# Performance work log

Measured on AMD Instinct MI355X. Metric: run time of the kernel, lower is better.

The kernel has to match this reference:

```python
import jax, jax.numpy as jnp
import numpy as np

POOL = 7          # pool_size (hard-coded 7x7 bin grid in source)
CROP = 2          # per-bin crop size: 14 // 7
ALPHA = 32        # channels per bin
H = W = 128
C = POOL * POOL * ALPHA  # 1568
NUM_ROIS = 4096


def setup_inputs() -> dict:
    key = jax.random.key(0)
    k_img, k_c, k_s = jax.random.split(key, 3)
    img = jax.random.normal(k_img, (1, H, W, C), dtype=jnp.float32)
    # valid normalized boxes [xmin, ymin, xmax, ymax] in [0, 1]
    cmin = jax.random.uniform(k_c, (1, NUM_ROIS, 2), dtype=jnp.float32) * 0.7
    size = 0.05 + jax.random.uniform(k_s, (1, NUM_ROIS, 2), dtype=jnp.float32) * 0.25
    rois = jnp.concatenate([cmin, cmin + size], axis=-1)  # (1, R, 4)
    return {"img": img, "rois": rois}


def _ps_roi_align(img, rois):
    # img: (1, H, W, 49*alpha) channels-last; rois: (1, R, 4) normalized xyxy
    h, w, c = img.shape[1], img.shape[2], img.shape[3]
    nbins = POOL * POOL
    alpha = c // nbins
    feat = img[0].reshape(h, w, nbins, alpha)  # channel group g <-> bin g

    xmin, ymin, xmax, ymax = (rois[0, :, i] for i in range(4))  # each (R,)
    step_y = (ymax - ymin) / POOL
    step_x = (xmax - xmin) / POOL

    g = jnp.arange(nbins)
    bx = (g // POOL).astype(img.dtype)  # bin order: bin_x outer, bin_y inner
    by = (g % POOL).astype(img.dtype)

    # per-roi per-bin sub-boxes, normalized coords, shape (R, B)
    y1 = ymin[:, None] + by[None, :] * step_y[:, None]
    x1 = xmin[:, None] + bx[None, :] * step_x[:, None]
    y2 = y1 + step_y[:, None]
    x2 = x1 + step_x[:, None]

    # tf.image.crop_and_resize sampling grid for crop size CROP (=2)
    t = jnp.arange(CROP, dtype=img.dtype) / (CROP - 1)  # (CROP,)
    ys = (y1[..., None] + (y2 - y1)[..., None] * t) * (h - 1)  # (R, B, CROP)
    xs = (x1[..., None] + (x2 - x1)[..., None] * t) * (w - 1)

    yg = ys[:, :, :, None]  # (R, B, CROP, 1)
    xg = xs[:, :, None, :]  # (R, B, 1, CROP)
    valid = (yg >= 0) & (yg <= h - 1) & (xg >= 0) & (xg <= w - 1)  # (R,B,CROP,CROP)

    y0f = jnp.floor(yg)
    x0f = jnp.floor(xg)
    wy = (yg - y0f)  # (R, B, CROP, 1)
    wx = (xg - x0f)  # (R, B, 1, CROP)

    y0 = jnp.clip(y0f.astype(jnp.int32), 0, h - 1)
    y1i = jnp.clip(y0 + 1, 0, h - 1)
    x0 = jnp.clip(x0f.astype(jnp.int32), 0, w - 1)
    x1i = jnp.clip(x0 + 1, 0, w - 1)

    bidx = g[None, :, None, None]  # (1, B, 1, 1) -> broadcasts with index grids

    def gather(yi, xi):
        yi, xi, bi = jnp.broadcast_arrays(yi, xi, bidx)
        return feat[yi, xi, bi]  # (R, B, CROP, CROP, alpha)

    val = (gather(y0, x0) * ((1 - wy) * (1 - wx))[..., None]
           + gather(y0, x1i) * ((1 - wy) * wx)[..., None]
           + gather(y1i, x0) * (wy * (1 - wx))[..., None]
           + gather(y1i, x1i) * (wy * wx)[..., None])
    val = jnp.where(valid[..., None], val, jnp.zeros((), img.dtype))

    pooled = val.max(axis=(2, 3))  # max over the CROPxCROP crop -> (R, B, alpha)
    return pooled.reshape(1, rois.shape[1], POOL, POOL, alpha)


def reference(img, rois):
    return _ps_roi_align(img, rois)
```

## Files before the change

### kernel.cpp

```cpp
#include <hip/hip_runtime.h>

#define POOLK 7
#define NBINS 49
#define ALPHA 32
#define C4N   8
#define HH    128
#define WW    128
#define NUM_ROIS 4096
#define F4_PER_PIX (NBINS * C4N)

__global__ __launch_bounds__(256) void psroi_align_kernel(
    const float* __restrict__ img,
    const float4* __restrict__ rois4,
    float4* __restrict__ out4)
{
    const int tid = blockIdx.x * blockDim.x + threadIdx.x;
    const int c4  = tid & (C4N - 1);
    const int rg  = tid >> 3;
    const int g   = rg % NBINS;
    const int roi = rg / NBINS;

    const float4 r = rois4[roi];

    const float step_x = (r.z - r.x) * (1.0f / POOLK);
    const float step_y = (r.w - r.y) * (1.0f / POOLK);

    const int p = g / POOLK;
    const int q = g % POOLK;

    const float x1 = r.x + (float)p * step_x;
    const float y1 = r.y + (float)q * step_y;

    const float scale = (float)(HH - 1);
    float ys[2], xs[2];
    ys[0] = y1 * scale;
    ys[1] = (y1 + step_y) * scale;
    xs[0] = x1 * scale;
    xs[1] = (x1 + step_x) * scale;

    float wy[2], wx[2];
    bool  vy[2], vx[2];
    int   yrow[4], xcol[4];
    #pragma unroll
    for (int s = 0; s < 2; ++s) {
        const float yg = ys[s];
        vy[s] = (yg >= 0.0f) && (yg <= (float)(HH - 1));
        const float y0f = floorf(yg);
        wy[s] = yg - y0f;
        int y0 = min(max((int)y0f, 0), HH - 1);
        yrow[2 * s]     = y0;
        yrow[2 * s + 1] = min(y0 + 1, HH - 1);

        const float xg = xs[s];
        vx[s] = (xg >= 0.0f) && (xg <= (float)(WW - 1));
        const float x0f = floorf(xg);
        wx[s] = xg - x0f;
        int x0 = min(max((int)x0f, 0), WW - 1);
        xcol[2 * s]     = x0;
        xcol[2 * s + 1] = min(x0 + 1, WW - 1);
    }

    const float4* __restrict__ feat = (const float4*)img;
    const int gbase = g * C4N + c4;

    int rowoff[4], coloff[4];
    #pragma unroll
    for (int i = 0; i < 4; ++i) {
        rowoff[i] = yrow[i] * (WW * F4_PER_PIX) + gbase;
        coloff[i] = xcol[i] * F4_PER_PIX;
    }

    float4 ld[16];
    #pragma unroll
    for (int rr = 0; rr < 4; ++rr) {
        #pragma unroll
        for (int cc = 0; cc < 4; ++cc) {
            ld[rr * 4 + cc] = feat[rowoff[rr] + coloff[cc]];
        }
    }

    float4 vmax;
    vmax.x = -INFINITY; vmax.y = -INFINITY; vmax.z = -INFINITY; vmax.w = -INFINITY;

    #pragma unroll
    for (int sy = 0; sy < 2; ++sy) {
        #pragma unroll
        for (int sx = 0; sx < 2; ++sx) {
            const float w11 = wy[sy] * wx[sx];
            const float w10 = wy[sy] - w11;
            const float w01 = wx[sx] - w11;
            const float w00 = 1.0f - wy[sy] - wx[sx] + w11;

            const float4 v00 = ld[(2 * sy)     * 4 + (2 * sx)];
            const float4 v01 = ld[(2 * sy)     * 4 + (2 * sx + 1)];
            const float4 v10 = ld[(2 * sy + 1) * 4 + (2 * sx)];
            const float4 v11 = ld[(2 * sy + 1) * 4 + (2 * sx + 1)];

            float4 v;
            v.x = v00.x * w00 + v01.x * w01 + v10.x * w10 + v11.x * w11;
            v.y = v00.y * w00 + v01.y * w01 + v10.y * w10 + v11.y * w11;
            v.z = v00.z * w00 + v01.z * w01 + v10.z * w10 + v11.z * w11;
            v.w = v00.w * w00 + v01.w * w01 + v10.w * w10 + v11.w * w11;

            if (!(vy[sy] && vx[sx])) { v.x = 0.0f; v.y = 0.0f; v.z = 0.0f; v.w = 0.0f; }

            vmax.x = fmaxf(vmax.x, v.x);
            vmax.y = fmaxf(vmax.y, v.y);
            vmax.z = fmaxf(vmax.z, v.z);
            vmax.w = fmaxf(vmax.w, v.w);
        }
    }

    out4[tid] = vmax;
}

extern "C" void kernel_launch(void* const* d_in, const int* in_sizes, int n_in,
                              void* d_out, int out_size, void* d_ws, size_t ws_size,
                              hipStream_t stream) {
    const float* img   = (const float*)d_in[0];
    const float4* rois = (const float4*)d_in[1];
    float4* out = (float4*)d_out;

    const int total_threads = NUM_ROIS * NBINS * C4N;
    const int block = 256;
    const int grid  = total_threads / block;
    psroi_align_kernel<<<grid, block, 0, stream>>>(img, rois, out);
}
```

Baseline: 183.2 us.

## Remap blocks so each XCD processes contiguous bin planes for L2 locality

Blocks are remapped so that each block handles 32 ROIs for a single bin group g. Blocks scheduled round-robin onto the same XCD cover consecutive bin planes, so each XCD's L2 only has to hold the feature-channel slices for about 6 bins rather than all 49. This targets L2 misses and cross-XCD duplication of the 100MB image. The cost is scattered output writes, since consecutive threads now write to different ROI rows, plus reliance on the round-robin block-to-XCD dispatch assumption.

New measurement: 165.0 us. 1.11x faster.

```diff
diff --git a/kernel.cpp b/kernel.cpp
--- a/kernel.cpp
+++ b/kernel.cpp
@@ -8,17 +8,24 @@
 #define WW    128
 #define NUM_ROIS 4096
 #define F4_PER_PIX (NBINS * C4N)
+#define NXCD 8
+#define SLOTS_PER_XCD 784
+#define CHUNKS_PER_PLANE 128
 
 __global__ __launch_bounds__(256) void psroi_align_kernel(
-    const float* __restrict__ img,
+    const float4* __restrict__ feat,
     const float4* __restrict__ rois4,
     float4* __restrict__ out4)
 {
-    const int tid = blockIdx.x * blockDim.x + threadIdx.x;
-    const int c4  = tid & (C4N - 1);
-    const int rg  = tid >> 3;
-    const int g   = rg % NBINS;
-    const int roi = rg / NBINS;
+    const int bid   = blockIdx.x;
+    const int xcd   = bid & (NXCD - 1);
+    const int j     = bid >> 3;
+    const int s     = xcd * SLOTS_PER_XCD + j;
+    const int g     = s >> 7;
+    const int chunk = s & (CHUNKS_PER_PLANE - 1);
+    const int t     = (chunk << 8) + threadIdx.x;
+    const int c4    = t & (C4N - 1);
+    const int roi   = t >> 3;
 
     const float4 r = rois4[roi];
 
@@ -42,25 +49,24 @@
     bool  vy[2], vx[2];
     int   yrow[4], xcol[4];
     #pragma unroll
-    for (int s = 0; s < 2; ++s) {
-        const float yg = ys[s];
-        vy[s] = (yg >= 0.0f) && (yg <= (float)(HH - 1));
+    for (int sa = 0; sa < 2; ++sa) {
+        const float yg = ys[sa];
+        vy[sa] = (yg >= 0.0f) && (yg <= (float)(HH - 1));
         const float y0f = floorf(yg);
-        wy[s] = yg - y0f;
+        wy[sa] = yg - y0f;
         int y0 = min(max((int)y0f, 0), HH - 1);
-        yrow[2 * s]     = y0;
-        yrow[2 * s + 1] = min(y0 + 1, HH - 1);
+        yrow[2 * sa]     = y0;
+        yrow[2 * sa + 1] = min(y0 + 1, HH - 1);
 
-        const float xg = xs[s];
-        vx[s] = (xg >= 0.0f) && (xg <= (float)(WW - 1));
+        const float xg = xs[sa];
+        vx[sa] = (xg >= 0.0f) && (xg <= (float)(WW - 1));
         const float x0f = floorf(xg);
-        wx[s] = xg - x0f;
+        wx[sa] = xg - x0f;
         int x0 = min(max((int)x0f, 0), WW - 1);
-        xcol[2 * s]     = x0;
-        xcol[2 * s + 1] = min(x0 + 1, WW - 1);
+        xcol[2 * sa]     = x0;
+        xcol[2 * sa + 1] = min(x0 + 1, WW - 1);
     }
 
-    const float4* __restrict__ feat = (const float4*)img;
     const int gbase = g * C4N + c4;
 
     int rowoff[4], coloff[4];
@@ -111,18 +117,16 @@
         }
     }
 
-    out4[tid] = vmax;
+    out4[(roi * NBINS + g) * C4N + c4] = vmax;
 }
 
 extern "C" void kernel_launch(void* const* d_in, const int* in_sizes, int n_in,
                               void* d_out, int out_size, void* d_ws, size_t ws_size,
                               hipStream_t stream) {
-    const float* img   = (const float*)d_in[0];
+    const float4* feat = (const float4*)d_in[0];
     const float4* rois = (const float4*)d_in[1];
     float4* out = (float4*)d_out;
 
-    const int total_threads = NUM_ROIS * NBINS * C4N;
-    const int block = 256;
-    const int grid  = total_threads / block;
-    psroi_align_kernel<<<grid, block, 0, stream>>>(img, rois, out);
+    const int grid = NXCD * SLOTS_PER_XCD;
+    psroi_align_kernel<<<grid, 256, 0, stream>>>(feat, rois, out);
 }
```
